# Kernel optimization log

Hardware: AMD Instinct MI355X
Metric: run time of the kernel (lower is better)

## Reference

```python
import jax, jax.numpy as jnp
import numpy as np


def _trilinear_sample(src, iz, iy, ix):
    """grid_sample 3D, mode='bilinear' (trilinear), padding_mode='zeros', on unnormalized voxel coords.
    src: [B,C,D,H,W]; iz,iy,ix: [B,D,H,W] float voxel coords (iz indexes D, iy H, ix W)."""
    B, C, D, H, W = src.shape
    z0 = jnp.floor(iz); y0 = jnp.floor(iy); x0 = jnp.floor(ix)
    tz = iz - z0; ty = iy - y0; tx = ix - x0
    z0i = z0.astype(jnp.int32); y0i = y0.astype(jnp.int32); x0i = x0.astype(jnp.int32)
    src_flat = src.reshape(B, C, D * H * W)

    def corner(dz, dy, dx):
        zc = z0i + dz; yc = y0i + dy; xc = x0i + dx
        valid = (zc >= 0) & (zc < D) & (yc >= 0) & (yc < H) & (xc >= 0) & (xc < W)
        zcc = jnp.clip(zc, 0, D - 1); ycc = jnp.clip(yc, 0, H - 1); xcc = jnp.clip(xc, 0, W - 1)
        lin = (zcc * H + ycc) * W + xcc                      # [B,D,H,W] flat spatial index
        vals = jax.vmap(lambda v, i: v[:, i.ravel()])(src_flat, lin)  # [B,C,D*H*W]
        vals = vals.reshape(B, C, D, H, W)
        wz = tz if dz else (1.0 - tz)
        wy = ty if dy else (1.0 - ty)
        wx = tx if dx else (1.0 - tx)
        w = (wz * wy * wx) * valid.astype(src.dtype)         # zeros padding
        return vals * w[:, None]

    out = jnp.zeros_like(src)
    for dz in (0, 1):
        for dy in (0, 1):
            for dx in (0, 1):
                out = out + corner(dz, dy, dx)
    return out


def reference(src, flow):
    B, _, D, H, W = flow.shape
    dt = flow.dtype
    # identity grid, channels ordered (z,y,x) i.e. (D,H,W), matching torch.meshgrid indexing='ij'
    gz, gy, gx = jnp.meshgrid(jnp.arange(D, dtype=dt), jnp.arange(H, dtype=dt),
                              jnp.arange(W, dtype=dt), indexing='ij')
    grid = jnp.stack([gz, gy, gx])[None]                     # [1,3,D,H,W]
    coords = grid + flow                                      # absolute voxel coords
    denom = jnp.array([D - 1, H - 1, W - 1], dtype=dt).reshape(1, 3, 1, 1, 1)
    norm = 2.0 * (coords / denom - 0.5)                       # normalized to [-1,1]
    # grid_sample expects last-dim order (x,y,z); align_corners=True unnormalization:
    ix = (norm[:, 2] + 1.0) * (W - 1) * 0.5
    iy = (norm[:, 1] + 1.0) * (H - 1) * 0.5
    iz = (norm[:, 0] + 1.0) * (D - 1) * 0.5
    return _trilinear_sample(src, iz, iy, ix)


def setup_inputs() -> dict:
    key = jax.random.key(0)
    k1, k2 = jax.random.split(key)
    B, C, D, H, W = 2, 2, 128, 160, 128
    src = jax.random.normal(k1, (B, C, D, H, W), dtype=jnp.float32)
    flow = jax.random.normal(k2, (B, 3, D, H, W), dtype=jnp.float32)
    return {"src": src, "flow": flow}
```

## Files before the change

### kernel.cpp

```cpp
#include <hip/hip_runtime.h>


#define B_ 2
#define C_ 2
#define D_ 128
#define H_ 160
#define W_ 128
constexpr int S_ = D_ * H_ * W_;

#define ZT 4
#define YT 8
#define XT 32
#define RZ 3
#define RY 3
#define RX 4
#define CZ (ZT + 2 * RZ)
#define CY (YT + 2 * RY)
#define CX (XT + 2 * RX)
#define PADP 41
#define NTHREADS 256
#define NQCHUNK (CZ * CY * (CX / 4))

__device__ __forceinline__ float2 compute_pair(
    int x, int y, int z, float fz, float fy, float fx,
    int zb, int yb, int xb,
    int zlo, int zhi, int ylo, int yhi, int xlo, int xhi,
    const float* __restrict__ tile, const float* __restrict__ s0)
{
    const float iz = (float)z + fz;
    const float iy = (float)y + fy;
    const float ix = (float)x + fx;

    const float zf = floorf(iz), yf = floorf(iy), xf = floorf(ix);
    const float tz = iz - zf, ty = iy - yf, tx = ix - xf;
    const int z0 = (int)zf, y0 = (int)yf, x0 = (int)xf;

    const int zc0 = min(max(z0, 0), D_ - 1), zc1 = min(max(z0 + 1, 0), D_ - 1);
    const int yc0 = min(max(y0, 0), H_ - 1), yc1 = min(max(y0 + 1, 0), H_ - 1);
    const int xp  = min(max(x0, 0), W_ - 2);

    const float wz0 = ((unsigned)z0       < (unsigned)D_) ? (1.f - tz) : 0.f;
    const float wz1 = ((unsigned)(z0 + 1) < (unsigned)D_) ? tz         : 0.f;
    const float wy0 = ((unsigned)y0       < (unsigned)H_) ? (1.f - ty) : 0.f;
    const float wy1 = ((unsigned)(y0 + 1) < (unsigned)H_) ? ty         : 0.f;
    const float wx0 = ((unsigned)x0       < (unsigned)W_) ? (1.f - tx) : 0.f;
    const float wx1 = ((unsigned)(x0 + 1) < (unsigned)W_) ? tx         : 0.f;
    const bool hi0 = x0 > xp;
    const bool lo1 = x0 < xp;

    const bool fast = (zc0 >= zlo) & (zc1 < zhi) &
                      (yc0 >= ylo) & (yc1 < yhi) &
                      (xp >= xlo) & (xp + 1 < xhi);

    float acc0, acc1;
    if (fast) {
        const int izl0 = zc0 - (zb - RZ), izl1 = zc1 - (zb - RZ);
        const int iyl0 = yc0 - (yb - RY), iyl1 = yc1 - (yb - RY);
        const int ixl  = xp - (xb - RX);
        const int o00 = ((izl0 * CY + iyl0) * PADP + ixl) * 2;
        const int o01 = ((izl0 * CY + iyl1) * PADP + ixl) * 2;
        const int o10 = ((izl1 * CY + iyl0) * PADP + ixl) * 2;
        const int o11 = ((izl1 * CY + iyl1) * PADP + ixl) * 2;
        const float2 a00 = *(const float2*)&tile[o00], b00 = *(const float2*)&tile[o00 + 2];
        const float2 a01 = *(const float2*)&tile[o01], b01 = *(const float2*)&tile[o01 + 2];
        const float2 a10 = *(const float2*)&tile[o10], b10 = *(const float2*)&tile[o10 + 2];
        const float2 a11 = *(const float2*)&tile[o11], b11 = *(const float2*)&tile[o11 + 2];
        const float q00 = wx0 * (hi0 ? b00.x : a00.x) + wx1 * (lo1 ? a00.x : b00.x);
        const float q01 = wx0 * (hi0 ? b01.x : a01.x) + wx1 * (lo1 ? a01.x : b01.x);
        const float q10 = wx0 * (hi0 ? b10.x : a10.x) + wx1 * (lo1 ? a10.x : b10.x);
        const float q11 = wx0 * (hi0 ? b11.x : a11.x) + wx1 * (lo1 ? a11.x : b11.x);
        const float r00 = wx0 * (hi0 ? b00.y : a00.y) + wx1 * (lo1 ? a00.y : b00.y);
        const float r01 = wx0 * (hi0 ? b01.y : a01.y) + wx1 * (lo1 ? a01.y : b01.y);
        const float r10 = wx0 * (hi0 ? b10.y : a10.y) + wx1 * (lo1 ? a10.y : b10.y);
        const float r11 = wx0 * (hi0 ? b11.y : a11.y) + wx1 * (lo1 ? a11.y : b11.y);
        acc0 = wz0 * (wy0 * q00 + wy1 * q01) + wz1 * (wy0 * q10 + wy1 * q11);
        acc1 = wz0 * (wy0 * r00 + wy1 * r01) + wz1 * (wy0 * r10 + wy1 * r11);
    } else {
        const int l00 = (zc0 * H_ + yc0) * W_ + xp;
        const int l01 = (zc0 * H_ + yc1) * W_ + xp;
        const int l10 = (zc1 * H_ + yc0) * W_ + xp;
        const int l11 = (zc1 * H_ + yc1) * W_ + xp;
        const float a00 = s0[l00],      b00 = s0[l00 + 1];
        const float a01 = s0[l01],      b01 = s0[l01 + 1];
        const float a10 = s0[l10],      b10 = s0[l10 + 1];
        const float a11 = s0[l11],      b11 = s0[l11 + 1];
        const float c00 = s0[S_ + l00], d00 = s0[S_ + l00 + 1];
        const float c01 = s0[S_ + l01], d01 = s0[S_ + l01 + 1];
        const float c10 = s0[S_ + l10], d10 = s0[S_ + l10 + 1];
        const float c11 = s0[S_ + l11], d11 = s0[S_ + l11 + 1];
        const float q00 = wx0 * (hi0 ? b00 : a00) + wx1 * (lo1 ? a00 : b00);
        const float q01 = wx0 * (hi0 ? b01 : a01) + wx1 * (lo1 ? a01 : b01);
        const float q10 = wx0 * (hi0 ? b10 : a10) + wx1 * (lo1 ? a10 : b10);
        const float q11 = wx0 * (hi0 ? b11 : a11) + wx1 * (lo1 ? a11 : b11);
        const float r00 = wx0 * (hi0 ? d00 : c00) + wx1 * (lo1 ? c00 : d00);
        const float r01 = wx0 * (hi0 ? d01 : c01) + wx1 * (lo1 ? c01 : d01);
        const float r10 = wx0 * (hi0 ? d10 : c10) + wx1 * (lo1 ? c10 : d10);
        const float r11 = wx0 * (hi0 ? d11 : c11) + wx1 * (lo1 ? c11 : d11);
        acc0 = wz0 * (wy0 * q00 + wy1 * q01) + wz1 * (wy0 * q10 + wy1 * q11);
        acc1 = wz0 * (wy0 * r00 + wy1 * r01) + wz1 * (wy0 * r10 + wy1 * r11);
    }
    return make_float2(acc0, acc1);
}

__global__ __launch_bounds__(NTHREADS, 4) void warp3d_tile(
    const float* __restrict__ src,
    const float* __restrict__ flow,
    float* __restrict__ out)
{
    __shared__ float tile[CZ * CY * PADP * 2];

    const int tid = threadIdx.x;
    const int xb = blockIdx.x * XT;
    const int yb = blockIdx.y * YT;
    const int bz = blockIdx.z;
    const int zb = (bz & 31) * ZT;
    const int b  = bz >> 5;

    const float* fb = flow + (long long)b * 3 * S_;
    const float* s0 = src + (long long)b * C_ * S_;
    float* o0       = out + (long long)b * C_ * S_;

#pragma unroll
    for (int j = 0; j < 6; ++j) {
        const int lin = j * NTHREADS + tid;
        if (lin < NQCHUNK) {
            const int row = lin / 10;
            const int c   = lin - row * 10;
            const int rz = row / CY, ry = row - rz * CY;
            const int gz = zb - RZ + rz;
            const int gy = yb - RY + ry;
            const int gx = xb - RX + c * 4;
            if ((unsigned)gz < (unsigned)D_ && (unsigned)gy < (unsigned)H_ &&
                (unsigned)gx <= (unsigned)(W_ - 4)) {
                const int off = (gz * H_ + gy) * W_ + gx;
                const float4 va = *(const float4*)(s0 + off);
                const float4 vb = *(const float4*)(s0 + S_ + off);
                float* dst = &tile[(row * PADP + c * 4) * 2];
                *(float4*)(dst)     = make_float4(va.x, vb.x, va.y, vb.y);
                *(float4*)(dst + 4) = make_float4(va.z, vb.z, va.w, vb.w);
            }
        }
    }
    __syncthreads();

    const int xq = tid & 7;
    const int ly = (tid >> 3) & 7;
    const int lz = tid >> 6;
    const int x0g = xb + xq * 4;
    const int y = yb + ly, z = zb + lz;
    const int sbase = (z * H_ + y) * W_ + x0g;

    const float4 fz4 = *(const float4*)(fb + sbase);
    const float4 fy4 = *(const float4*)(fb + S_ + sbase);
    const float4 fx4 = *(const float4*)(fb + 2 * S_ + sbase);

    const int zlo = max(0, zb - RZ), zhi = min(D_, zb + ZT + RZ);
    const int ylo = max(0, yb - RY), yhi = min(H_, yb + YT + RY);
    const int xlo = max(0, xb - RX), xhi = min(W_, xb + XT + RX);

    const float2 v0 = compute_pair(x0g + 0, y, z, fz4.x, fy4.x, fx4.x,
                                   zb, yb, xb, zlo, zhi, ylo, yhi, xlo, xhi, tile, s0);
    const float2 v1 = compute_pair(x0g + 1, y, z, fz4.y, fy4.y, fx4.y,
                                   zb, yb, xb, zlo, zhi, ylo, yhi, xlo, xhi, tile, s0);
    const float2 v2 = compute_pair(x0g + 2, y, z, fz4.z, fy4.z, fx4.z,
                                   zb, yb, xb, zlo, zhi, ylo, yhi, xlo, xhi, tile, s0);
    const float2 v3 = compute_pair(x0g + 3, y, z, fz4.w, fy4.w, fx4.w,
                                   zb, yb, xb, zlo, zhi, ylo, yhi, xlo, xhi, tile, s0);

    *(float4*)(o0 + sbase)      = make_float4(v0.x, v1.x, v2.x, v3.x);
    *(float4*)(o0 + S_ + sbase) = make_float4(v0.y, v1.y, v2.y, v3.y);
}

extern "C" void kernel_launch(void* const* d_in, const int* in_sizes, int n_in,
                              void* d_out, int out_size, void* d_ws, size_t ws_size,
                              hipStream_t stream) {
    const float* src  = (const float*)d_in[0];
    const float* flow = (const float*)d_in[1];
    float* out = (float*)d_out;

    dim3 grid(W_ / XT, H_ / YT, (D_ / ZT) * B_);
    warp3d_tile<<<grid, NTHREADS, 0, stream>>>(src, flow, out);
}
```

Baseline: 162.2 us.

## Load source halo directly into LDS with larger z-tile and planar layout

Doubles the z-tile to 8 and the block to 512 threads, which shrinks the ratio of halo to interior for the shared-memory source tile. The tile is now filled with direct global-to-LDS 16-byte loads on clamped coordinates, replacing the register round trip and the channel interleave. The layout becomes two planar channel planes instead of interleaved float2 pairs. Flow loads are issued before the barrier so they overlap the tile fill; the larger tile raises LDS use per block and may limit occupancy.

```diff
diff --git a/kernel.cpp b/kernel.cpp
--- a/kernel.cpp
+++ b/kernel.cpp
@@ -8,7 +8,7 @@
 #define W_ 128
 constexpr int S_ = D_ * H_ * W_;
 
-#define ZT 4
+#define ZT 8
 #define YT 8
 #define XT 32
 #define RZ 3
@@ -17,9 +17,17 @@
 #define CZ (ZT + 2 * RZ)
 #define CY (YT + 2 * RY)
 #define CX (XT + 2 * RX)
-#define PADP 41
-#define NTHREADS 256
-#define NQCHUNK (CZ * CY * (CX / 4))
+#define NTHREADS 512
+#define PLANE (CZ * CY * CX)
+#define CHPP (PLANE / 4)
+#define NCHUNK_TOT (2 * CHPP)
+
+typedef const __attribute__((address_space(1))) unsigned int ga_u32;
+typedef __attribute__((address_space(3))) unsigned int lds_u32;
+
+__device__ __forceinline__ void gload16(const float* g, float* l) {
+    __builtin_amdgcn_global_load_lds((ga_u32*)g, (lds_u32*)l, 16, 0, 0);
+}
 
 __device__ __forceinline__ float2 compute_pair(
     int x, int y, int z, float fz, float fy, float fx,
@@ -57,22 +65,26 @@
         const int izl0 = zc0 - (zb - RZ), izl1 = zc1 - (zb - RZ);
         const int iyl0 = yc0 - (yb - RY), iyl1 = yc1 - (yb - RY);
         const int ixl  = xp - (xb - RX);
-        const int o00 = ((izl0 * CY + iyl0) * PADP + ixl) * 2;
-        const int o01 = ((izl0 * CY + iyl1) * PADP + ixl) * 2;
-        const int o10 = ((izl1 * CY + iyl0) * PADP + ixl) * 2;
-        const int o11 = ((izl1 * CY + iyl1) * PADP + ixl) * 2;
-        const float2 a00 = *(const float2*)&tile[o00], b00 = *(const float2*)&tile[o00 + 2];
-        const float2 a01 = *(const float2*)&tile[o01], b01 = *(const float2*)&tile[o01 + 2];
-        const float2 a10 = *(const float2*)&tile[o10], b10 = *(const float2*)&tile[o10 + 2];
-        const float2 a11 = *(const float2*)&tile[o11], b11 = *(const float2*)&tile[o11 + 2];
-        const float q00 = wx0 * (hi0 ? b00.x : a00.x) + wx1 * (lo1 ? a00.x : b00.x);
-        const float q01 = wx0 * (hi0 ? b01.x : a01.x) + wx1 * (lo1 ? a01.x : b01.x);
-        const float q10 = wx0 * (hi0 ? b10.x : a10.x) + wx1 * (lo1 ? a10.x : b10.x);
-        const float q11 = wx0 * (hi0 ? b11.x : a11.x) + wx1 * (lo1 ? a11.x : b11.x);
-        const float r00 = wx0 * (hi0 ? b00.y : a00.y) + wx1 * (lo1 ? a00.y : b00.y);
-        const float r01 = wx0 * (hi0 ? b01.y : a01.y) + wx1 * (lo1 ? a01.y : b01.y);
-        const float r10 = wx0 * (hi0 ? b10.y : a10.y) + wx1 * (lo1 ? a10.y : b10.y);
-        const float r11 = wx0 * (hi0 ? b11.y : a11.y) + wx1 * (lo1 ? a11.y : b11.y);
+        const int o00 = (izl0 * CY + iyl0) * CX + ixl;
+        const int o01 = (izl0 * CY + iyl1) * CX + ixl;
+        const int o10 = (izl1 * CY + iyl0) * CX + ixl;
+        const int o11 = (izl1 * CY + iyl1) * CX + ixl;
+        const float a00 = tile[o00],         b00 = tile[o00 + 1];
+        const float a01 = tile[o01],         b01 = tile[o01 + 1];
+        const float a10 = tile[o10],         b10 = tile[o10 + 1];
+        const float a11 = tile[o11],         b11 = tile[o11 + 1];
+        const float c00 = tile[PLANE + o00], d00 = tile[PLANE + o00 + 1];
+        const float c01 = tile[PLANE + o01], d01 = tile[PLANE + o01 + 1];
+        const float c10 = tile[PLANE + o10], d10 = tile[PLANE + o10 + 1];
+        const float c11 = tile[PLANE + o11], d11 = tile[PLANE + o11 + 1];
+        const float q00 = wx0 * (hi0 ? b00 : a00) + wx1 * (lo1 ? a00 : b00);
+        const float q01 = wx0 * (hi0 ? b01 : a01) + wx1 * (lo1 ? a01 : b01);
+        const float q10 = wx0 * (hi0 ? b10 : a10) + wx1 * (lo1 ? a10 : b10);
+        const float q11 = wx0 * (hi0 ? b11 : a11) + wx1 * (lo1 ? a11 : b11);
+        const float r00 = wx0 * (hi0 ? d00 : c00) + wx1 * (lo1 ? c00 : d00);
+        const float r01 = wx0 * (hi0 ? d01 : c01) + wx1 * (lo1 ? c01 : d01);
+        const float r10 = wx0 * (hi0 ? d10 : c10) + wx1 * (lo1 ? c10 : d10);
+        const float r11 = wx0 * (hi0 ? d11 : c11) + wx1 * (lo1 ? c11 : d11);
         acc0 = wz0 * (wy0 * q00 + wy1 * q01) + wz1 * (wy0 * q10 + wy1 * q11);
         acc1 = wz0 * (wy0 * r00 + wy1 * r01) + wz1 * (wy0 * r10 + wy1 * r11);
     } else {
@@ -107,41 +119,34 @@
     const float* __restrict__ flow,
     float* __restrict__ out)
 {
-    __shared__ float tile[CZ * CY * PADP * 2];
+    __shared__ float tile[2 * PLANE];
 
     const int tid = threadIdx.x;
     const int xb = blockIdx.x * XT;
     const int yb = blockIdx.y * YT;
     const int bz = blockIdx.z;
-    const int zb = (bz & 31) * ZT;
-    const int b  = bz >> 5;
+    const int zb = (bz & 15) * ZT;
+    const int b  = bz >> 4;
 
     const float* fb = flow + (long long)b * 3 * S_;
     const float* s0 = src + (long long)b * C_ * S_;
     float* o0       = out + (long long)b * C_ * S_;
 
 #pragma unroll
-    for (int j = 0; j < 6; ++j) {
+    for (int j = 0; j < 8; ++j) {
         const int lin = j * NTHREADS + tid;
-        if (lin < NQCHUNK) {
-            const int row = lin / 10;
-            const int c   = lin - row * 10;
+        if (lin < NCHUNK_TOT) {
+            const int pl  = (lin >= CHPP) ? 1 : 0;
+            const int rem = lin - pl * CHPP;
+            const int row = rem / 10;
+            const int cq  = rem - row * 10;
             const int rz = row / CY, ry = row - rz * CY;
-            const int gz = zb - RZ + rz;
-            const int gy = yb - RY + ry;
-            const int gx = xb - RX + c * 4;
-            if ((unsigned)gz < (unsigned)D_ && (unsigned)gy < (unsigned)H_ &&
-                (unsigned)gx <= (unsigned)(W_ - 4)) {
-                const int off = (gz * H_ + gy) * W_ + gx;
-                const float4 va = *(const float4*)(s0 + off);
-                const float4 vb = *(const float4*)(s0 + S_ + off);
-                float* dst = &tile[(row * PADP + c * 4) * 2];
-                *(float4*)(dst)     = make_float4(va.x, vb.x, va.y, vb.y);
-                *(float4*)(dst + 4) = make_float4(va.z, vb.z, va.w, vb.w);
-            }
+            const int gz = min(max(zb - RZ + rz, 0), D_ - 1);
+            const int gy = min(max(yb - RY + ry, 0), H_ - 1);
+            const int gx = min(max(xb - RX + cq * 4, 0), W_ - 4);
+            gload16(s0 + pl * S_ + (gz * H_ + gy) * W_ + gx, &tile[lin * 4]);
         }
     }
-    __syncthreads();
 
     const int xq = tid & 7;
     const int ly = (tid >> 3) & 7;
@@ -149,10 +154,11 @@
     const int x0g = xb + xq * 4;
     const int y = yb + ly, z = zb + lz;
     const int sbase = (z * H_ + y) * W_ + x0g;
-
     const float4 fz4 = *(const float4*)(fb + sbase);
     const float4 fy4 = *(const float4*)(fb + S_ + sbase);
     const float4 fx4 = *(const float4*)(fb + 2 * S_ + sbase);
+
+    __syncthreads();
 
     const int zlo = max(0, zb - RZ), zhi = min(D_, zb + ZT + RZ);
     const int ylo = max(0, yb - RY), yhi = min(H_, yb + YT + RY);
```

New measurement: 153.2 us, median of 2. -5.5%, faster.
